# Kernel optimization log

Hardware: AMD Instinct MI355X
Metric: run time of the kernel (lower is better)

The kernel has to match this reference:

```python
import jax, jax.numpy as jnp
import numpy as np
from jax import lax

B = 4096          # graphs in batch
NPG = 50          # nodes per graph
N = B * NPG       # 204800 nodes
E = N * 8         # 1638400 directed edges
F_IN = 128
H = 64            # GCN hidden
K = 10            # SortPooling k
NUM_CLASSES = 10


def _glorot(key, shape):
    lim = float(np.sqrt(6.0 / (shape[0] + shape[1])))
    return jax.random.uniform(key, shape, jnp.float32, -lim, lim)


def setup_inputs() -> dict:
    key = jax.random.key(0)
    ks = jax.random.split(key, 10)
    x = jax.random.normal(ks[0], (N, F_IN), jnp.float32)
    edge_index = jax.random.randint(ks[1], (2, E), 0, N)
    batch = jnp.repeat(jnp.arange(B), NPG)  # sorted graph ids, 50 nodes each
    return {
        "x": x, "edge_index": edge_index, "batch": batch,
        "W1": _glorot(ks[2], (F_IN, H)), "b1": jnp.zeros((H,), jnp.float32),
        "W2": _glorot(ks[3], (H, H)), "b2": jnp.zeros((H,), jnp.float32),
        "W3": _glorot(ks[4], (H, H)), "b3": jnp.zeros((H,), jnp.float32),
        "Wc1": jax.random.normal(ks[5], (32, K, 4), jnp.float32) * 0.05,
        "bc1": jnp.zeros((32,), jnp.float32),
        "Wc2": jax.random.normal(ks[6], (64, 32, 3), jnp.float32) * 0.05,
        "bc2": jnp.zeros((64,), jnp.float32),
        "Wf": _glorot(ks[7], (H, NUM_CLASSES)),
        "bf": jnp.zeros((NUM_CLASSES,), jnp.float32),
    }


def reference(x, edge_index, batch, W1, b1, W2, b2, W3, b3, Wc1, bc1, Wc2, bc2, Wf, bf):
    row, col = edge_index[0], edge_index[1]
    # PyG GCNConv normalization with self-loops: deg over targets + 1
    deg = jax.ops.segment_sum(jnp.ones((E,), jnp.float32), col, num_segments=N) + 1.0
    dinv = lax.rsqrt(deg)
    ecoef = (dinv[row] * dinv[col])[:, None]   # [E,1] edge norm
    scoef = (dinv * dinv)[:, None]             # [N,1] self-loop norm

    def gcn(h, W, b):
        h = h @ W
        agg = jax.ops.segment_sum(h[row] * ecoef, col, num_segments=N) + h * scoef
        return agg + b

    x1 = jnp.tanh(gcn(x, W1, b1))
    x2 = jnp.tanh(gcn(x1, W2, b2))
    x3 = jnp.tanh(gcn(x2, W3, b3))
    feat = jnp.concatenate([x1, x2, x3], axis=-1)   # JK cat -> [N, 192]

    # DGL SortPooling(k=10): sort each node's features ascending, then take
    # top-k nodes per graph by the last (largest) feature, descending.
    feat = jnp.sort(feat, axis=-1)
    order = jnp.lexsort((-feat[:, -1], batch))      # graph asc, key desc
    fs, bs = feat[order], batch[order]
    counts = jax.ops.segment_sum(jnp.ones((N,), jnp.int32), batch, num_segments=B)
    starts = jnp.cumsum(counts) - counts
    rank = jnp.arange(N) - starts[bs]               # within-graph rank
    mask = (rank < K)[:, None]
    pooled = jnp.zeros((B, K, feat.shape[-1]), feat.dtype)
    pooled = pooled.at[bs, jnp.minimum(rank, K - 1)].add(jnp.where(mask, fs, 0.0))

    h = pooled  # [B, 10, 192] == x.view(B, 10, 192)
    h = lax.conv_general_dilated(h, Wc1, (4,), 'VALID',
                                 dimension_numbers=('NCH', 'OIH', 'NCH')) + bc1[None, :, None]
    h = jax.nn.relu(h)                              # [B,32,48]
    h = lax.reduce_window(h, -jnp.inf, lax.max, (1, 1, 4), (1, 1, 4), 'VALID')  # [B,32,12]
    h = lax.conv_general_dilated(h, Wc2, (3,), 'VALID',
                                 dimension_numbers=('NCH', 'OIH', 'NCH')) + bc2[None, :, None]
    h = jax.nn.relu(h)                              # [B,64,4]
    h = lax.reduce_window(h, -jnp.inf, lax.max, (1, 1, 4), (1, 1, 4), 'VALID')  # [B,64,1]
    xf = h.reshape(B, -1)                           # [B,64]
    c = jax.nn.relu(xf) @ Wf + bf                   # [B,num_classes]
    return (c, xf)
```

## Files before the change

### kernel.cpp

```cpp
#include <hip/hip_runtime.h>
#include <hip/hip_bf16.h>

#define NN 204800
#define EE 1638400
#define BBATCH 4096
#define NPGRAPH 50
#define KTOP 10
#define NBLK 200

#define OFF_W1  0
#define OFF_W2  8192
#define OFF_W3  12288
#define OFF_B1  16384
#define OFF_B2  16448
#define OFF_B3  16512
#define OFF_WC1 16576
#define OFF_BC1 17856
#define OFF_WC2 17888
#define OFF_BC2 24032
#define OFF_WF  24096
#define OFF_BF  24736
#define WTOT    24746

__device__ __forceinline__ float bf2f(unsigned short u) {
    unsigned int x = ((unsigned int)u) << 16;
    float f; __builtin_memcpy(&f, &x, 4); return f;
}

__device__ __forceinline__ long long pack_sc(int s, float c) {
    return ((long long)(unsigned)__float_as_int(c) << 32) | (unsigned)s;
}

__global__ void detect_kernel(const unsigned int* __restrict__ xw,
                              const unsigned int* __restrict__ eiw,
                              int* __restrict__ flags) {
    __shared__ int s_f32, s_i64;
    int t = threadIdx.x;
    if (t == 0) { s_f32 = 0; s_i64 = 1; }
    __syncthreads();
    unsigned w = xw[t];
    unsigned u0 = w & 0xffffu, u1 = w >> 16;
    int e0 = (u0 >> 7) & 0xff, e1 = (u1 >> 7) & 0xff;
    if (e0 >= 0x88 || e1 >= 0x88) atomicOr(&s_f32, 1);
    if (eiw[2 * t + 1] != 0) atomicAnd(&s_i64, 0);
    __syncthreads();
    if (t == 0) { flags[0] = s_f32; flags[1] = s_i64; }
}


struct WPtrs { const void* p[12]; };

__global__ void convert_weights_kernel(WPtrs wp, const int* __restrict__ flags,
                                       float* __restrict__ dst) {
    const int lens[12] = {8192,4096,4096,64,64,64,1280,32,6144,64,640,10};
    const int offs[12] = {OFF_W1,OFF_W2,OFF_W3,OFF_B1,OFF_B2,OFF_B3,
                          OFF_WC1,OFF_BC1,OFF_WC2,OFF_BC2,OFF_WF,OFF_BF};
    int f32 = flags[0];
    int t = blockIdx.x * 256 + threadIdx.x;
    for (int s = 0; s < 12; ++s) {
        if (t < lens[s]) {
            float v = f32 ? ((const float*)wp.p[s])[t]
                          : bf2f(((const unsigned short*)wp.p[s])[t]);
            dst[offs[s] + t] = v;
            return;
        }
        t -= lens[s];
    }
}


__global__ void zero_int_kernel(int* p, int n) {
    int i = blockIdx.x * 256 + threadIdx.x;
    if (i < n) p[i] = 0;
}

__device__ __forceinline__ int ld_idx(const void* ei, int i64, long pos) {
    return i64 ? (int)((const long long*)ei)[pos] : ((const int*)ei)[pos];
}

__global__ void count_kernel(const void* __restrict__ ei, const int* __restrict__ flags,
                             int* __restrict__ cnt) {
    int e = blockIdx.x * 256 + threadIdx.x;
    if (e >= EE) return;
    int c = ld_idx(ei, flags[1], (long)EE + e);
    atomicAdd(&cnt[c], 1);
}

__global__ __launch_bounds__(1024) void scan1_kernel(const int* __restrict__ cnt,
                                                     int* __restrict__ offs,
                                                     float* __restrict__ dinv,
                                                     int* __restrict__ blksum) {
    __shared__ int wsum[16];
    int b = blockIdx.x, t = threadIdx.x;
    int lane = t & 63, wid = t >> 6;
    int i = b * 1024 + t;
    int v = cnt[i] + 1;
    int x = v;
    #pragma unroll
    for (int d = 1; d < 64; d <<= 1) { int y = __shfl_up(x, d, 64); if (lane >= d) x += y; }
    if (lane == 63) wsum[wid] = x;
    __syncthreads();
    if (t == 0) {
        int run = 0;
        #pragma unroll
        for (int k = 0; k < 16; ++k) { int tmp = wsum[k]; wsum[k] = run; run += tmp; }
        blksum[b] = run;
    }
    __syncthreads();
    offs[i] = wsum[wid] + x - v;
    dinv[i] = (float)(1.0 / sqrt((double)v));
}

__global__ __launch_bounds__(256) void scan2_kernel(int* __restrict__ blksum) {
    __shared__ int wsum[4];
    int t = threadIdx.x, lane = t & 63, wid = t >> 6;
    int v = (t < NBLK) ? blksum[t] : 0;
    int x = v;
    #pragma unroll
    for (int d = 1; d < 64; d <<= 1) { int y = __shfl_up(x, d, 64); if (lane >= d) x += y; }
    if (lane == 63) wsum[wid] = x;
    __syncthreads();
    int pre = 0;
    for (int k = 0; k < wid; ++k) pre += wsum[k];
    if (t < NBLK) blksum[t] = pre + x - v;
}

__global__ __launch_bounds__(1024) void scan3_kernel(int* __restrict__ offs,
                                                     const int* __restrict__ blksum) {
    int b = blockIdx.x, i = b * 1024 + threadIdx.x;
    offs[i] += blksum[b];
    if (i == 0) offs[NN] = EE + NN;
}

__global__ void fill_self_kernel(const int* __restrict__ offs, const float* __restrict__ dinv,
                                 int* __restrict__ cursor, long long* __restrict__ epack) {
    int n = blockIdx.x * 256 + threadIdx.x;
    if (n >= NN) return;
    int p = offs[n];
    float d = dinv[n];
    __builtin_nontemporal_store(pack_sc(n, d * d), &epack[p]);
    cursor[n] = 1;
}

__global__ void fill_edges_kernel(const void* __restrict__ ei, const int* __restrict__ flags,
                                  const int* __restrict__ offs,
                                  const float* __restrict__ dinv, int* __restrict__ cursor,
                                  long long* __restrict__ epack) {
    int e = blockIdx.x * 256 + threadIdx.x;
    if (e >= EE) return;
    int i64 = flags[1];
    int r = ld_idx(ei, i64, e);
    int c = ld_idx(ei, i64, (long)EE + e);
    int p = offs[c] + atomicAdd(&cursor[c], 1);
    __builtin_nontemporal_store(pack_sc(r, dinv[r] * dinv[c]), &epack[p]);
}


template<int KD, int MODE>
__global__ __launch_bounds__(256) void xw_kernel(const void* __restrict__ xin_,
                                                 const int* __restrict__ flags,
                                                 int row_stride, int col_off,
                                                 const float* __restrict__ W,
                                                 float* __restrict__ hout) {
    __shared__ float xs[2][128 * 33];
    const int t = threadIdx.x;
    const int row = t & 127;
    const int cgs = __builtin_amdgcn_readfirstlane(t >> 7);
    const long row0 = (long)blockIdx.x * 128;
    const bool bf16in = (MODE == 1) && (flags[0] == 0);

    float acc[32];
    #pragma unroll
    for (int c = 0; c < 32; ++c) acc[c] = 0.f;

    if (bf16in) {
        const unsigned short* xg = (const unsigned short*)xin_;
        unsigned short* xsh = (unsigned short*)&xs[0][0];
        for (int kb = 0; kb < KD; kb += 32) {
            __syncthreads();
            #pragma unroll
            for (int u = 0; u < 16; ++u) {
                int idx = u * 256 + t;
                int r = idx >> 5, k = idx & 31;
                xsh[r * 66 + k] = xg[(row0 + r) * row_stride + col_off + kb + k];
            }
            __syncthreads();
            const unsigned short* xrow = xsh + row * 66;
            const float* wb = W + (long)kb * 64 + cgs * 32;
            #pragma unroll 2
            for (int k = 0; k < 32; ++k) {
                float xk = bf2f(xrow[k]);
                const float* wr = wb + (long)k * 64;
                #pragma unroll
                for (int c = 0; c < 32; ++c) acc[c] = fmaf(xk, wr[c], acc[c]);
            }
        }
    } else {
        const float* xg = (const float*)xin_;
        float4 rg[4];
        #pragma unroll
        for (int u = 0; u < 4; ++u) {
            int f4 = u * 256 + t;
            int r = f4 >> 3, k4 = f4 & 7;
            rg[u] = *(const float4*)(xg + (row0 + r) * row_stride + col_off + k4 * 4);
        }
        int cur = 0;
        for (int kb = 0; kb < KD; kb += 32) {
            #pragma unroll
            for (int u = 0; u < 4; ++u) {
                int f4 = u * 256 + t;
                int r = f4 >> 3, k4 = f4 & 7;
                float* d = &xs[cur][r * 33 + k4 * 4];
                d[0] = rg[u].x; d[1] = rg[u].y; d[2] = rg[u].z; d[3] = rg[u].w;
            }
            if (kb + 32 < KD) {
                #pragma unroll
                for (int u = 0; u < 4; ++u) {
                    int f4 = u * 256 + t;
                    int r = f4 >> 3, k4 = f4 & 7;
                    rg[u] = *(const float4*)(xg + (row0 + r) * row_stride + col_off + kb + 32 + k4 * 4);
                }
            }
            __syncthreads();
            const float* xrow = &xs[cur][row * 33];
            const float* wb = W + (long)kb * 64 + cgs * 32;
            #pragma unroll 2
            for (int k = 0; k < 32; ++k) {
                float xk = xrow[k];
                const float* wr = wb + (long)k * 64;
                #pragma unroll
                for (int c = 0; c < 32; ++c) acc[c] = fmaf(xk, wr[c], acc[c]);
            }
            cur ^= 1;
        }
    }

    float* o = hout + (row0 + row) * 64 + cgs * 32;
    #pragma unroll
    for (int c = 0; c < 32; c += 4) {
        float4 v; v.x = acc[c]; v.y = acc[c+1]; v.z = acc[c+2]; v.w = acc[c+3];
        *(float4*)(o + c) = v;
    }
}


__global__ __launch_bounds__(256) void spmm_kernel(const float* __restrict__ h,
                                                   const int* __restrict__ offs,
                                                   const long long* __restrict__ epack,
                                                   const float* __restrict__ bias,
                                                   float* __restrict__ featOut,
                                                   float* __restrict__ keyOut) {
    int node = blockIdx.x * 4 + (threadIdx.x >> 6);
    int lane = threadIdx.x & 63;
    int j0 = offs[node], j1 = offs[node + 1];
    float acc = 0.f;

    for (int base = j0; base < j1; base += 64) {
        int n = j1 - base; if (n > 64) n = 64;
        long long my = 0;
        if (lane < n) my = epack[base + lane];

        int m = 0;
        for (; m + 8 <= n; m += 8) {
            float hv[8], cf[8];
            #pragma unroll
            for (int u = 0; u < 8; ++u) {
                long long e = __shfl(my, m + u, 64);
                int s = (int)(unsigned)e;
                cf[u] = __int_as_float((int)(e >> 32));
                hv[u] = h[(long)s * 64 + lane];
            }
            #pragma unroll
            for (int u = 0; u < 8; ++u) acc = fmaf(hv[u], cf[u], acc);
        }
        for (; m < n; ++m) {
            long long e = __shfl(my, m, 64);
            int s = (int)(unsigned)e;
            float cf = __int_as_float((int)(e >> 32));
            acc = fmaf(h[(long)s * 64 + lane], cf, acc);
        }
    }

    float val = tanhf(acc + bias[lane]);
    featOut[(long)node * 192 + lane] = val;
    float m = val;
    #pragma unroll
    for (int d = 32; d; d >>= 1) m = fmaxf(m, __shfl_xor(m, d, 64));
    if (lane == 0) keyOut[node] = m;
}


__global__ __launch_bounds__(256) void select_topk_kernel(const float* __restrict__ key3,
                                                          int* __restrict__ topidx) {
    int g = blockIdx.x * 4 + (threadIdx.x >> 6);
    int lane = threadIdx.x & 63;
    int node = g * NPGRAPH + lane;
    float k = -INFINITY;
    if (lane < NPGRAPH)
        k = fmaxf(fmaxf(key3[node], key3[NN + node]), key3[2 * NN + node]);
    for (int r = 0; r < KTOP; ++r) {
        float bk = k; int bi = lane;
        #pragma unroll
        for (int d = 32; d; d >>= 1) {
            float ok = __shfl_xor(bk, d, 64);
            int   oi = __shfl_xor(bi, d, 64);
            if (ok > bk || (ok == bk && oi < bi)) { bk = ok; bi = oi; }
        }
        if (lane == 0) topidx[g * KTOP + r] = g * NPGRAPH + bi;
        if (lane == bi) k = -INFINITY;
    }
}


__global__ __launch_bounds__(256) void sort_gather_kernel(const float* __restrict__ feat,
                                                          const int* __restrict__ topidx,
                                                          float* __restrict__ pooled) {
    int lane = threadIdx.x & 63;
    int w = threadIdx.x >> 6;
    int slot = blockIdx.x * 4 + w;
    int node = topidx[slot];

    unsigned v[4];
    #pragma unroll
    for (int t = 0; t < 3; ++t) {
        float x = feat[(long)node * 192 + 64 * t + lane];
        unsigned u = __float_as_uint(x);
        v[t] = (u & 0x80000000u) ? ~u : (u | 0x80000000u);
    }
    v[3] = 0xFF800000u;

    #pragma unroll
    for (int k = 2; k <= 256; k <<= 1) {
        #pragma unroll
        for (int d = 128; d >= 1; d >>= 1) {
            if (d >= k) continue;
            if (d >= 64) {
                int dt = d >> 6;
                #pragma unroll
                for (int t = 0; t < 4; ++t) {
                    if (!(t & dt)) {
                        int t2 = t | dt;
                        bool asc = ((64 * t) & k) == 0;
                        unsigned a = v[t], b = v[t2];
                        unsigned mn = a < b ? a : b;
                        unsigned mx = a < b ? b : a;
                        v[t]  = asc ? mn : mx;
                        v[t2] = asc ? mx : mn;
                    }
                }
            } else {
                #pragma unroll
                for (int t = 0; t < 4; ++t) {
                    unsigned p = (unsigned)__shfl_xor((int)v[t], d, 64);
                    int e = 64 * t + lane;
                    bool lower = (lane & d) == 0;
                    bool asc = (e & k) == 0;
                    unsigned mn = v[t] < p ? v[t] : p;
                    unsigned mx = v[t] < p ? p : v[t];
                    v[t] = (lower == asc) ? mn : mx;
                }
            }
        }
    }

    #pragma unroll
    for (int t = 0; t < 3; ++t) {
        unsigned kk = v[t];
        unsigned u = (kk & 0x80000000u) ? (kk ^ 0x80000000u) : ~kk;
        pooled[(long)slot * 192 + 64 * t + lane] = __uint_as_float(u);
    }
}


__global__ __launch_bounds__(256) void conv1_kernel(const float* __restrict__ pooled,
                                                    const float* __restrict__ wc,
                                                    float* __restrict__ pool1) {
    __shared__ float p[1920];
    __shared__ float w[1280];
    __shared__ float c1[1536];
    int b = blockIdx.x, t = threadIdx.x;
    for (int i = t; i < 1920; i += 256) p[i] = pooled[(long)b * 1920 + i];
    for (int i = t; i < 1280; i += 256) w[i] = wc[OFF_WC1 + i];
    __syncthreads();
    for (int o = t; o < 1536; o += 256) {
        int oc = o / 48, s = o % 48;
        float acc = wc[OFF_BC1 + oc];
        #pragma unroll
        for (int ic = 0; ic < 10; ++ic)
            #pragma unroll
            for (int t4 = 0; t4 < 4; ++t4)
                acc = fmaf(p[ic * 192 + s * 4 + t4], w[oc * 40 + ic * 4 + t4], acc);
        c1[o] = fmaxf(acc, 0.f);
    }
    __syncthreads();
    for (int o = t; o < 384; o += 256) {
        int oc = o / 12, q = o % 12;
        float m = c1[oc * 48 + q * 4];
        #pragma unroll
        for (int u = 1; u < 4; ++u) m = fmaxf(m, c1[oc * 48 + q * 4 + u]);
        pool1[(long)b * 384 + o] = m;
    }
}


__global__ __launch_bounds__(256) void conv2_fc_kernel(const float* __restrict__ pool1,
                                                       const float* __restrict__ wc,
                                                       const int* __restrict__ flags,
                                                       void* __restrict__ outv) {
    __shared__ float p[384];
    __shared__ float w2[6144];
    __shared__ float r2[256];
    __shared__ float xfs[64];
    int b = blockIdx.x, t = threadIdx.x;
    int f32o = flags[0];
    for (int i = t; i < 384; i += 256) p[i] = pool1[(long)b * 384 + i];
    for (int i = t; i < 6144; i += 256) w2[i] = wc[OFF_WC2 + i];
    __syncthreads();
    {
        int oc = t >> 2, s = t & 3;
        float acc = wc[OFF_BC2 + oc];
        #pragma unroll
        for (int ic = 0; ic < 32; ++ic)
            #pragma unroll
            for (int t3 = 0; t3 < 3; ++t3)
                acc = fmaf(p[ic * 12 + 3 * s + t3], w2[oc * 96 + ic * 3 + t3], acc);
        r2[t] = fmaxf(acc, 0.f);
    }
    __syncthreads();
    if (t < 64) {
        float m = fmaxf(fmaxf(r2[4*t], r2[4*t+1]), fmaxf(r2[4*t+2], r2[4*t+3]));
        xfs[t] = m;
        long idx = (long)BBATCH * 10 + (long)b * 64 + t;
        if (f32o) ((float*)outv)[idx] = m;
        else      ((__hip_bfloat16*)outv)[idx] = __float2bfloat16(m);
    }
    __syncthreads();
    if (t < 10) {
        float acc = wc[OFF_BF + t];
        #pragma unroll
        for (int o = 0; o < 64; ++o)
            acc = fmaf(fmaxf(xfs[o], 0.f), wc[OFF_WF + o * 10 + t], acc);
        long idx = (long)b * 10 + t;
        if (f32o) ((float*)outv)[idx] = acc;
        else      ((__hip_bfloat16*)outv)[idx] = __float2bfloat16(acc);
    }
}


extern "C" void kernel_launch(void* const* d_in, const int* in_sizes, int n_in,
                              void* d_out, int out_size, void* d_ws, size_t ws_size,
                              hipStream_t stream) {
    const void* x  = d_in[0];
    const void* ei = d_in[1];
    WPtrs wp;
    wp.p[0] = d_in[3];
    wp.p[1] = d_in[5];
    wp.p[2] = d_in[7];
    wp.p[3] = d_in[4];
    wp.p[4] = d_in[6];
    wp.p[5] = d_in[8];
    wp.p[6] = d_in[9];
    wp.p[7] = d_in[10];
    wp.p[8] = d_in[11];
    wp.p[9] = d_in[12];
    wp.p[10] = d_in[13];
    wp.p[11] = d_in[14];

    char* ws = (char*)d_ws;
    size_t o = 0;
    auto take = [&](size_t bytes) { char* r = ws + o; o = (o + bytes + 255) & ~(size_t)255; return r; };
    int*       flags  = (int*)      take(2 * 4);
    float*     wconv  = (float*)    take((size_t)WTOT * 4);
    int*       offs   = (int*)      take((size_t)(NN + 1) * 4);
    long long* epack  = (long long*)take((size_t)(EE + NN) * 8);
    float*     key3   = (float*)    take((size_t)3 * NN * 4);
    int*       topidx = (int*)      take((size_t)BBATCH * KTOP * 4);
    int*       blksum = (int*)      take((size_t)NBLK * 4);
    char*      hbase  = take((size_t)NN * 64 * 4);
    float*     feat   = (float*)    take((size_t)NN * 192 * 4);

    float* h      = (float*)hbase;
    int*   cnt    = (int*)(hbase);
    int*   cursor = (int*)(hbase + (1u << 20));
    float* dinv   = (float*)(hbase + (2u << 20));
    float* pooled = (float*)(hbase);
    float* pool1  = (float*)(hbase + (34u << 20));

    detect_kernel<<<1, 256, 0, stream>>>((const unsigned int*)x, (const unsigned int*)ei, flags);
    convert_weights_kernel<<<(WTOT + 255) / 256, 256, 0, stream>>>(wp, flags, wconv);
    zero_int_kernel<<<NN / 256, 256, 0, stream>>>(cnt, NN);
    count_kernel<<<EE / 256, 256, 0, stream>>>(ei, flags, cnt);
    scan1_kernel<<<NBLK, 1024, 0, stream>>>(cnt, offs, dinv, blksum);
    scan2_kernel<<<1, 256, 0, stream>>>(blksum);
    scan3_kernel<<<NBLK, 1024, 0, stream>>>(offs, blksum);
    fill_self_kernel<<<NN / 256, 256, 0, stream>>>(offs, dinv, cursor, epack);
    fill_edges_kernel<<<EE / 256, 256, 0, stream>>>(ei, flags, offs, dinv, cursor, epack);

    xw_kernel<128, 1><<<NN / 128, 256, 0, stream>>>(x, flags, 128, 0, wconv + OFF_W1, h);
    spmm_kernel<<<NN / 4, 256, 0, stream>>>(h, offs, epack, wconv + OFF_B1, feat, key3);
    xw_kernel<64, 0><<<NN / 128, 256, 0, stream>>>(feat, flags, 192, 0, wconv + OFF_W2, h);
    spmm_kernel<<<NN / 4, 256, 0, stream>>>(h, offs, epack, wconv + OFF_B2, feat + 64, key3 + NN);
    xw_kernel<64, 0><<<NN / 128, 256, 0, stream>>>(feat, flags, 192, 64, wconv + OFF_W3, h);
    spmm_kernel<<<NN / 4, 256, 0, stream>>>(h, offs, epack, wconv + OFF_B3, feat + 128, key3 + 2 * NN);

    select_topk_kernel<<<BBATCH / 4, 256, 0, stream>>>(key3, topidx);
    sort_gather_kernel<<<BBATCH * KTOP / 4, 256, 0, stream>>>(feat, topidx, pooled);
    conv1_kernel<<<BBATCH, 256, 0, stream>>>(pooled, wconv, pool1);
    conv2_fc_kernel<<<BBATCH, 256, 0, stream>>>(pool1, wconv, flags, d_out);
}
```

Measured before the change: 879.4 us.

## Process two nodes per wavefront in SpMM with interleaved edge gathers

The SpMM kernel now has each 64-lane wavefront aggregate two consecutive destination nodes at once. It walks both edge lists in chunks of four and issues the gathers for the two nodes together to raise memory-level parallelism. Every lane now loads the packed edge entries directly (a broadcast load) instead of doing one coalesced load followed by shuffles. The grid is halved to match. The cost is fewer wavefronts, more registers per thread, and divergent loop trip counts when the two nodes have different degrees.

```diff
diff --git a/kernel.cpp b/kernel.cpp
--- a/kernel.cpp
+++ b/kernel.cpp
@@ -250,43 +250,58 @@
                                                    const float* __restrict__ bias,
                                                    float* __restrict__ featOut,
                                                    float* __restrict__ keyOut) {
-    int node = blockIdx.x * 4 + (threadIdx.x >> 6);
+    int wid = blockIdx.x * 4 + (threadIdx.x >> 6);
     int lane = threadIdx.x & 63;
-    int j0 = offs[node], j1 = offs[node + 1];
-    float acc = 0.f;
-
-    for (int base = j0; base < j1; base += 64) {
-        int n = j1 - base; if (n > 64) n = 64;
-        long long my = 0;
-        if (lane < n) my = epack[base + lane];
-
-        int m = 0;
-        for (; m + 8 <= n; m += 8) {
-            float hv[8], cf[8];
-            #pragma unroll
-            for (int u = 0; u < 8; ++u) {
-                long long e = __shfl(my, m + u, 64);
-                int s = (int)(unsigned)e;
-                cf[u] = __int_as_float((int)(e >> 32));
-                hv[u] = h[(long)s * 64 + lane];
-            }
-            #pragma unroll
-            for (int u = 0; u < 8; ++u) acc = fmaf(hv[u], cf[u], acc);
-        }
-        for (; m < n; ++m) {
-            long long e = __shfl(my, m, 64);
-            int s = (int)(unsigned)e;
-            float cf = __int_as_float((int)(e >> 32));
-            acc = fmaf(h[(long)s * 64 + lane], cf, acc);
-        }
-    }
-
-    float val = tanhf(acc + bias[lane]);
-    featOut[(long)node * 192 + lane] = val;
-    float m = val;
-    #pragma unroll
-    for (int d = 32; d; d >>= 1) m = fmaxf(m, __shfl_xor(m, d, 64));
-    if (lane == 0) keyOut[node] = m;
+    int n0 = wid * 2;
+
+    int ja = offs[n0];
+    int ea_end = offs[n0 + 1];
+    int jb = ea_end;
+    int eb_end = offs[n0 + 2];
+
+    float acc0 = 0.f, acc1 = 0.f;
+    float bv = bias[lane];
+
+    while (ja < ea_end || jb < eb_end) {
+        int na = ea_end - ja; na = na > 4 ? 4 : na;
+        int nb = eb_end - jb; nb = nb > 4 ? 4 : nb;
+
+        long long ra[4], rb[4];
+        #pragma unroll
+        for (int u = 0; u < 4; ++u) if (u < na) ra[u] = epack[ja + u];
+        #pragma unroll
+        for (int u = 0; u < 4; ++u) if (u < nb) rb[u] = epack[jb + u];
+
+        float hva[4], hvb[4];
+        #pragma unroll
+        for (int u = 0; u < 4; ++u)
+            if (u < na) hva[u] = h[(long)(int)(unsigned)ra[u] * 64 + lane];
+        #pragma unroll
+        for (int u = 0; u < 4; ++u)
+            if (u < nb) hvb[u] = h[(long)(int)(unsigned)rb[u] * 64 + lane];
+
+        #pragma unroll
+        for (int u = 0; u < 4; ++u)
+            if (u < na) acc0 = fmaf(hva[u], __int_as_float((int)(ra[u] >> 32)), acc0);
+        #pragma unroll
+        for (int u = 0; u < 4; ++u)
+            if (u < nb) acc1 = fmaf(hvb[u], __int_as_float((int)(rb[u] >> 32)), acc1);
+
+        ja += na; jb += nb;
+    }
+
+    float v0 = tanhf(acc0 + bv);
+    float v1 = tanhf(acc1 + bv);
+    featOut[(long)n0 * 192 + lane] = v0;
+    featOut[(long)(n0 + 1) * 192 + lane] = v1;
+
+    float m0 = v0, m1 = v1;
+    #pragma unroll
+    for (int d = 32; d; d >>= 1) {
+        m0 = fmaxf(m0, __shfl_xor(m0, d, 64));
+        m1 = fmaxf(m1, __shfl_xor(m1, d, 64));
+    }
+    if (lane == 0) { keyOut[n0] = m0; keyOut[n0 + 1] = m1; }
 }
 
 
@@ -497,11 +512,11 @@
     fill_edges_kernel<<<EE / 256, 256, 0, stream>>>(ei, flags, offs, dinv, cursor, epack);
 
     xw_kernel<128, 1><<<NN / 128, 256, 0, stream>>>(x, flags, 128, 0, wconv + OFF_W1, h);
-    spmm_kernel<<<NN / 4, 256, 0, stream>>>(h, offs, epack, wconv + OFF_B1, feat, key3);
+    spmm_kernel<<<NN / 8, 256, 0, stream>>>(h, offs, epack, wconv + OFF_B1, feat, key3);
     xw_kernel<64, 0><<<NN / 128, 256, 0, stream>>>(feat, flags, 192, 0, wconv + OFF_W2, h);
-    spmm_kernel<<<NN / 4, 256, 0, stream>>>(h, offs, epack, wconv + OFF_B2, feat + 64, key3 + NN);
+    spmm_kernel<<<NN / 8, 256, 0, stream>>>(h, offs, epack, wconv + OFF_B2, feat + 64, key3 + NN);
     xw_kernel<64, 0><<<NN / 128, 256, 0, stream>>>(feat, flags, 192, 64, wconv + OFF_W3, h);
-    spmm_kernel<<<NN / 4, 256, 0, stream>>>(h, offs, epack, wconv + OFF_B3, feat + 128, key3 + 2 * NN);
+    spmm_kernel<<<NN / 8, 256, 0, stream>>>(h, offs, epack, wconv + OFF_B3, feat + 128, key3 + 2 * NN);
 
     select_topk_kernel<<<BBATCH / 4, 256, 0, stream>>>(key3, topidx);
     sort_gather_kernel<<<BBATCH * KTOP / 4, 256, 0, stream>>>(feat, topidx, pooled);
```

New measurement: 979.6 us. 1.11x slower.

## Fuse layer-2/3 GEMM into SpMM via aggregate-then-transform ordering

Applied to the files above, without the earlier changes.

Layers 2 and 3 now aggregate neighbour features straight from the feature buffer (stride 192) and then apply the 64x64 weight inside the SpMM kernel through a per-node wave-level GEMV built on shuffles. Because A(XW) equals (AX)W, the separate xw_kernel launches and the intermediate h buffer writes and reads go away. The cost is gathering from a strided 192-wide buffer, which has poorer cache-line locality, plus 64 shuffles and weight reads per node. The kernel reads and writes the same feat buffer, but in disjoint column ranges.

```diff
diff --git a/kernel.cpp b/kernel.cpp
--- a/kernel.cpp
+++ b/kernel.cpp
@@ -244,9 +244,11 @@
 }
 
 
-__global__ __launch_bounds__(256) void spmm_kernel(const float* __restrict__ h,
+template<int GEMV, int IST, int IOFF, int OOFF>
+__global__ __launch_bounds__(256) void spmm_kernel(const float* __restrict__ hin,
                                                    const int* __restrict__ offs,
                                                    const long long* __restrict__ epack,
+                                                   const float* __restrict__ W,
                                                    const float* __restrict__ bias,
                                                    float* __restrict__ featOut,
                                                    float* __restrict__ keyOut) {
@@ -268,7 +270,7 @@
                 long long e = __shfl(my, m + u, 64);
                 int s = (int)(unsigned)e;
                 cf[u] = __int_as_float((int)(e >> 32));
-                hv[u] = h[(long)s * 64 + lane];
+                hv[u] = hin[(long)s * IST + IOFF + lane];
             }
             #pragma unroll
             for (int u = 0; u < 8; ++u) acc = fmaf(hv[u], cf[u], acc);
@@ -277,12 +279,24 @@
             long long e = __shfl(my, m, 64);
             int s = (int)(unsigned)e;
             float cf = __int_as_float((int)(e >> 32));
-            acc = fmaf(h[(long)s * 64 + lane], cf, acc);
-        }
-    }
-
-    float val = tanhf(acc + bias[lane]);
-    featOut[(long)node * 192 + lane] = val;
+            acc = fmaf(hin[(long)s * IST + IOFF + lane], cf, acc);
+        }
+    }
+
+    float val;
+    if (GEMV) {
+        float g = 0.f;
+        #pragma unroll
+        for (int k = 0; k < 64; ++k) {
+            float ak = __shfl(acc, k, 64);
+            g = fmaf(ak, W[k * 64 + lane], g);
+        }
+        val = tanhf(g + bias[lane]);
+    } else {
+        val = tanhf(acc + bias[lane]);
+    }
+
+    featOut[(long)node * 192 + OOFF + lane] = val;
     float m = val;
     #pragma unroll
     for (int d = 32; d; d >>= 1) m = fmaxf(m, __shfl_xor(m, d, 64));
@@ -497,11 +511,12 @@
     fill_edges_kernel<<<EE / 256, 256, 0, stream>>>(ei, flags, offs, dinv, cursor, epack);
 
     xw_kernel<128, 1><<<NN / 128, 256, 0, stream>>>(x, flags, 128, 0, wconv + OFF_W1, h);
-    spmm_kernel<<<NN / 4, 256, 0, stream>>>(h, offs, epack, wconv + OFF_B1, feat, key3);
-    xw_kernel<64, 0><<<NN / 128, 256, 0, stream>>>(feat, flags, 192, 0, wconv + OFF_W2, h);
-    spmm_kernel<<<NN / 4, 256, 0, stream>>>(h, offs, epack, wconv + OFF_B2, feat + 64, key3 + NN);
-    xw_kernel<64, 0><<<NN / 128, 256, 0, stream>>>(feat, flags, 192, 64, wconv + OFF_W3, h);
-    spmm_kernel<<<NN / 4, 256, 0, stream>>>(h, offs, epack, wconv + OFF_B3, feat + 128, key3 + 2 * NN);
+    spmm_kernel<0, 64, 0, 0><<<NN / 4, 256, 0, stream>>>(h, offs, epack, nullptr,
+                                                         wconv + OFF_B1, feat, key3);
+    spmm_kernel<1, 192, 0, 64><<<NN / 4, 256, 0, stream>>>(feat, offs, epack, wconv + OFF_W2,
+                                                           wconv + OFF_B2, feat, key3 + NN);
+    spmm_kernel<1, 192, 64, 128><<<NN / 4, 256, 0, stream>>>(feat, offs, epack, wconv + OFF_W3,
+                                                             wconv + OFF_B3, feat, key3 + 2 * NN);
 
     select_topk_kernel<<<BBATCH / 4, 256, 0, stream>>>(key3, topidx);
     sort_gather_kernel<<<BBATCH * KTOP / 4, 256, 0, stream>>>(feat, topidx, pooled);
```

After: 969.0 us. 10.2% more time.

## Fuse layer-2/3 feature transform into SpMM via aggregate-then-multiply reordering

Applied to the files above, without the earlier changes.

For GCN layers 2 and 3, the kernel now aggregates the previous layer's 64-wide features over neighbours first, then multiplies by W in-register using wave shuffles, replacing the separate xw_kernel launches. This drops two GEMM kernels and the write and re-read of the intermediate h buffer. The cost is that gathers now read rows with a 192-float stride from the feat array rather than a packed 64-wide buffer, and each wave does a 64x64 GEMV per node with W read from global/L1.

```diff
diff --git a/kernel.cpp b/kernel.cpp
--- a/kernel.cpp
+++ b/kernel.cpp
@@ -244,12 +244,12 @@
 }
 
 
-__global__ __launch_bounds__(256) void spmm_kernel(const float* __restrict__ h,
-                                                   const int* __restrict__ offs,
-                                                   const long long* __restrict__ epack,
-                                                   const float* __restrict__ bias,
-                                                   float* __restrict__ featOut,
-                                                   float* __restrict__ keyOut) {
+__global__ __launch_bounds__(256) void spmm1_kernel(const float* __restrict__ h,
+                                                    const int* __restrict__ offs,
+                                                    const long long* __restrict__ epack,
+                                                    const float* __restrict__ bias,
+                                                    float* __restrict__ featOut,
+                                                    float* __restrict__ keyOut) {
     int node = blockIdx.x * 4 + (threadIdx.x >> 6);
     int lane = threadIdx.x & 63;
     int j0 = offs[node], j1 = offs[node + 1];
@@ -283,6 +283,67 @@
 
     float val = tanhf(acc + bias[lane]);
     featOut[(long)node * 192 + lane] = val;
+    float m = val;
+    #pragma unroll
+    for (int d = 32; d; d >>= 1) m = fmaxf(m, __shfl_xor(m, d, 64));
+    if (lane == 0) keyOut[node] = m;
+}
+
+
+template<int IOFF, int OOFF>
+__global__ __launch_bounds__(256) void spmm_gemv_kernel(const float* __restrict__ hin,
+                                                        const int* __restrict__ offs,
+                                                        const long long* __restrict__ epack,
+                                                        const float* __restrict__ W,
+                                                        const float* __restrict__ bias,
+                                                        float* __restrict__ featOut,
+                                                        float* __restrict__ keyOut) {
+    int node = blockIdx.x * 4 + (threadIdx.x >> 6);
+    int lane = threadIdx.x & 63;
+    int j0 = offs[node], j1 = offs[node + 1];
+    float acc = 0.f;
+
+    for (int base = j0; base < j1; base += 64) {
+        int n = j1 - base; if (n > 64) n = 64;
+        long long my = 0;
+        if (lane < n) my = epack[base + lane];
+
+        int m = 0;
+        for (; m + 8 <= n; m += 8) {
+            float hv[8], cf[8];
+            #pragma unroll
+            for (int u = 0; u < 8; ++u) {
+                long long e = __shfl(my, m + u, 64);
+                int s = (int)(unsigned)e;
+                cf[u] = __int_as_float((int)(e >> 32));
+                hv[u] = hin[(long)s * 192 + IOFF + lane];
+            }
+            #pragma unroll
+            for (int u = 0; u < 8; ++u) acc = fmaf(hv[u], cf[u], acc);
+        }
+        for (; m < n; ++m) {
+            long long e = __shfl(my, m, 64);
+            int s = (int)(unsigned)e;
+            float cf = __int_as_float((int)(e >> 32));
+            acc = fmaf(hin[(long)s * 192 + IOFF + lane], cf, acc);
+        }
+    }
+
+    float g[8];
+    #pragma unroll
+    for (int b = 0; b < 8; ++b) {
+        float ak[8];
+        #pragma unroll
+        for (int u = 0; u < 8; ++u) ak[u] = __shfl(acc, b * 8 + u, 64);
+        float s = 0.f;
+        #pragma unroll
+        for (int u = 0; u < 8; ++u) s = fmaf(ak[u], W[(b * 8 + u) * 64 + lane], s);
+        g[b] = s;
+    }
+    float gg = ((g[0] + g[1]) + (g[2] + g[3])) + ((g[4] + g[5]) + (g[6] + g[7]));
+    float val = tanhf(gg + bias[lane]);
+
+    featOut[(long)node * 192 + OOFF + lane] = val;
     float m = val;
     #pragma unroll
     for (int d = 32; d; d >>= 1) m = fmaxf(m, __shfl_xor(m, d, 64));
@@ -497,11 +558,11 @@
     fill_edges_kernel<<<EE / 256, 256, 0, stream>>>(ei, flags, offs, dinv, cursor, epack);
 
     xw_kernel<128, 1><<<NN / 128, 256, 0, stream>>>(x, flags, 128, 0, wconv + OFF_W1, h);
-    spmm_kernel<<<NN / 4, 256, 0, stream>>>(h, offs, epack, wconv + OFF_B1, feat, key3);
-    xw_kernel<64, 0><<<NN / 128, 256, 0, stream>>>(feat, flags, 192, 0, wconv + OFF_W2, h);
-    spmm_kernel<<<NN / 4, 256, 0, stream>>>(h, offs, epack, wconv + OFF_B2, feat + 64, key3 + NN);
-    xw_kernel<64, 0><<<NN / 128, 256, 0, stream>>>(feat, flags, 192, 64, wconv + OFF_W3, h);
-    spmm_kernel<<<NN / 4, 256, 0, stream>>>(h, offs, epack, wconv + OFF_B3, feat + 128, key3 + 2 * NN);
+    spmm1_kernel<<<NN / 4, 256, 0, stream>>>(h, offs, epack, wconv + OFF_B1, feat, key3);
+    spmm_gemv_kernel<0, 64><<<NN / 4, 256, 0, stream>>>(feat, offs, epack, wconv + OFF_W2,
+                                                        wconv + OFF_B2, feat, key3 + NN);
+    spmm_gemv_kernel<64, 128><<<NN / 4, 256, 0, stream>>>(feat, offs, epack, wconv + OFF_W3,
+                                                          wconv + OFF_B3, feat, key3 + 2 * NN);
 
     select_topk_kernel<<<BBATCH / 4, 256, 0, stream>>>(key3, topidx);
     sort_gather_kernel<<<BBATCH * KTOP / 4, 256, 0, stream>>>(feat, topidx, pooled);
```

After: 974.6 us (median of 2 runs). +10.8%, slower.
